# Kernel tuning notes

Hardware: AMD Instinct MI355X
Metric: run time of the kernel (lower is better)

Reference implementation:

```python
import jax, jax.numpy as jnp
import numpy as np

N_NODES = 50000
N_EDGES = 800000
IN_F, OUT_F = 128, 128
NUM_HEADS, QUERY_DIM = 3, 8


def setup_inputs() -> dict:
    key = jax.random.key(0)
    ks = jax.random.split(key, 8)
    scale = 1.0 / np.sqrt(IN_F)
    return {
        "x": jax.random.normal(ks[0], (N_NODES, IN_F), dtype=jnp.float32),
        "adj": jax.random.randint(ks[1], (2, N_EDGES), 0, N_NODES, dtype=jnp.int64),
        "Wq": jax.random.normal(ks[2], (QUERY_DIM * NUM_HEADS, IN_F), dtype=jnp.float32) * scale,
        "bq": jax.random.normal(ks[3], (QUERY_DIM * NUM_HEADS,), dtype=jnp.float32) * 0.01,
        "aw": jax.random.normal(ks[4], (NUM_HEADS, 2 * QUERY_DIM * NUM_HEADS), dtype=jnp.float32) * 0.1,
        "ab": jax.random.normal(ks[5], (NUM_HEADS,), dtype=jnp.float32) * 0.01,
        "lw": jax.random.normal(ks[6], (OUT_F, IN_F), dtype=jnp.float32) * scale,
        "lb": jax.random.normal(ks[7], (OUT_F,), dtype=jnp.float32) * 0.01,
    }


def reference(x, adj, Wq, bq, aw, ab, lw, lb):
    n = x.shape[0]
    s, r = adj[0], adj[1]
    # per-node query features: [N, H*Q]
    attr = x @ Wq.T + bq
    # per-edge attention logits from concat(sender, receiver): [E, H]
    e = jnp.concatenate((attr[s], attr[r]), axis=1) @ aw.T + ab
    # segment softmax over incoming edges of each receiver
    seg_max = jax.ops.segment_max(e, r, num_segments=n)  # [N, H]
    e = jnp.exp(e - jax.lax.stop_gradient(seg_max)[r])
    denom = jax.ops.segment_sum(e, r, num_segments=n)  # [N, H]
    alpha = e / jnp.maximum(denom[r], 1e-16)  # [E, H]
    # node value projection and attention-weighted aggregation
    h = x @ lw.T + lb  # [N, OUT_F]
    msg = h[s] * alpha.mean(axis=1, keepdims=True)  # [E, OUT_F]
    out = jax.ops.segment_sum(msg, r, num_segments=n)  # [N, OUT_F]
    return jax.nn.silu(out)
```

## Files before the change

kernel.cpp:

```cpp
#include <hip/hip_runtime.h>
#include <hip/hip_fp16.h>
#include <math.h>

#define N_NODES 50000
#define N_EDGES 800000
#define IN_F 128
#define OUT_F 128
#define NH 3
#define SCAN_NB ((N_NODES + 255) / 256)
#define NODE_NB ((N_NODES + 31) / 32)
#define NBH 32
#define EPB (N_EDGES / NBH)
#define QNODES (N_NODES / 4)
#define CQ_BLOCKS (NBH * 4)

typedef __attribute__((ext_vector_type(8))) _Float16 f16x8;
typedef __attribute__((ext_vector_type(4))) float f32x4;

__global__ __launch_bounds__(256) void weights_kernel(
    const float* __restrict__ Wq, const float* __restrict__ bq,
    const float* __restrict__ aw, const float* __restrict__ ab,
    const float* __restrict__ lw,
    _Float16* __restrict__ w2h, float* __restrict__ b2,
    _Float16* __restrict__ lwh, int* __restrict__ sync)
{
    int t = blockIdx.x * 256 + threadIdx.x;
    if (blockIdx.x == 0 && threadIdx.x < 8) sync[threadIdx.x] = 0;
    if (t < 16 * 128) {
        int prow = t >> 7;
        int i    = t & 127;
        int r = -1;
        if (prow < 3) r = prow;
        else if (prow >= 4 && prow < 7) r = prow - 1;
        if (r < 0) {
            w2h[prow * 128 + i] = (_Float16)0.0f;
        } else {
            int hh  = (r < 3) ? r : r - 3;
            int off = (r < 3) ? 0 : 24;
            const float* awr = aw + hh * 48 + off;
            float acc = 0.0f;
            #pragma unroll
            for (int q = 0; q < 24; q++) acc += awr[q] * Wq[q * 128 + i];
            w2h[prow * 128 + i] = (_Float16)acc;
            if (i == 0) {
                float b = 0.0f;
                #pragma unroll
                for (int q = 0; q < 24; q++) b += awr[q] * bq[q];
                if (r >= 3) b += ab[hh];
                b2[r] = b;
            }
        }
    }
    int u = t - 16 * 128;
    if (u >= 0 && u < 128 * 128) lwh[u] = (_Float16)lw[u];
}

__global__ __launch_bounds__(256) void node_count_kernel(
    const float* __restrict__ x, const _Float16* __restrict__ lwh,
    const float* __restrict__ lb, const _Float16* __restrict__ w2h,
    const float* __restrict__ b2, const int* __restrict__ adj,
    __half* __restrict__ h, float* __restrict__ as4, float* __restrict__ ar4,
    unsigned int* __restrict__ hist, unsigned short* __restrict__ rank)
{
    __shared__ __align__(16) unsigned int shmem[QNODES / 2];

    if (blockIdx.x < CQ_BLOCKS) {
        unsigned int* cnt = shmem;
        for (int i = threadIdx.x; i < QNODES / 2; i += 256) cnt[i] = 0;
        __syncthreads();
        const int c = blockIdx.x >> 2, q = blockIdx.x & 3;
        const int nlo = q * QNODES;
        const int e0 = c * EPB, e1 = e0 + EPB;
        for (int base = e0 + threadIdx.x; base < e1; base += 8 * 256) {
            int rs[8];
            #pragma unroll
            for (int u = 0; u < 8; u++) {
                int e = base + u * 256;
                rs[u] = (e < e1) ? adj[N_EDGES + e] : -1;
            }
            #pragma unroll
            for (int u = 0; u < 8; u++) {
                int e = base + u * 256;
                int lr = rs[u] - nlo;
                if ((unsigned)lr < (unsigned)QNODES) {
                    int sh = (lr & 1) * 16;
                    unsigned int old = atomicAdd(&cnt[lr >> 1], 1u << sh);
                    rank[e] = (unsigned short)(old >> sh);
                }
            }
        }
        __syncthreads();
        unsigned int* hb = hist + (size_t)c * (N_NODES / 2) + q * (QNODES / 2);
        for (int i = threadIdx.x; i < QNODES / 2; i += 256)
            hb[i] = cnt[i];
        return;
    }

    unsigned char* xs = (unsigned char*)shmem;
    const int tx = threadIdx.x;
    const int nb = (blockIdx.x - CQ_BLOCKS) * 32;

    #pragma unroll
    for (int it = 0; it < 2; it++) {
        int cc = it * 256 + tx;
        int node = cc >> 4, kc = cc & 15;
        int gn = nb + node;
        f16x8 v;
        if (gn < N_NODES) {
            const float4* xr = (const float4*)(x + (size_t)gn * 128 + kc * 8);
            float4 p = xr[0], qq = xr[1];
            v[0] = (_Float16)p.x;  v[1] = (_Float16)p.y;
            v[2] = (_Float16)p.z;  v[3] = (_Float16)p.w;
            v[4] = (_Float16)qq.x; v[5] = (_Float16)qq.y;
            v[6] = (_Float16)qq.z; v[7] = (_Float16)qq.w;
        } else {
            #pragma unroll
            for (int e = 0; e < 8; e++) v[e] = (_Float16)0.0f;
        }
        int byte = node * 256 + ((kc * 16) ^ ((node & 7) << 4));
        *(f16x8*)(xs + byte) = v;
    }
    __syncthreads();

    const int wave = tx >> 6, lane = tx & 63;
    const int l15 = lane & 15, lg = lane >> 4;

    f16x8 afr[2][4];
    #pragma unroll
    for (int m = 0; m < 2; m++) {
        int out = wave * 32 + m * 16 + l15;
        const f16x8* ar8 = (const f16x8*)(lwh + (size_t)out * 128);
        #pragma unroll
        for (int kk = 0; kk < 4; kk++)
            afr[m][kk] = ar8[kk * 4 + lg];
    }
    f16x8 a6[4];
    {
        const f16x8* w8 = (const f16x8*)(w2h + (size_t)l15 * 128);
        #pragma unroll
        for (int kk = 0; kk < 4; kk++) a6[kk] = w8[kk * 4 + lg];
    }

    f32x4 acc[2][2], acc6[2];
    #pragma unroll
    for (int m = 0; m < 2; m++)
        #pragma unroll
        for (int n = 0; n < 2; n++)
            acc[m][n] = (f32x4){0.f, 0.f, 0.f, 0.f};
    #pragma unroll
    for (int n = 0; n < 2; n++) acc6[n] = (f32x4){0.f, 0.f, 0.f, 0.f};

    #pragma unroll
    for (int kk = 0; kk < 4; kk++) {
        f16x8 bfr[2];
        #pragma unroll
        for (int n = 0; n < 2; n++) {
            int node = n * 16 + l15;
            int byte = node * 256 + ((kk * 64 + lg * 16) ^ ((node & 7) << 4));
            bfr[n] = *(const f16x8*)(xs + byte);
        }
        #pragma unroll
        for (int m = 0; m < 2; m++)
            #pragma unroll
            for (int n = 0; n < 2; n++)
                acc[m][n] = __builtin_amdgcn_mfma_f32_16x16x32_f16(
                    afr[m][kk], bfr[n], acc[m][n], 0, 0, 0);
        if (wave == 0) {
            #pragma unroll
            for (int n = 0; n < 2; n++)
                acc6[n] = __builtin_amdgcn_mfma_f32_16x16x32_f16(
                    a6[kk], bfr[n], acc6[n], 0, 0, 0);
        }
    }

    #pragma unroll
    for (int n = 0; n < 2; n++) {
        int gn = nb + n * 16 + l15;
        if (gn >= N_NODES) continue;
        #pragma unroll
        for (int m = 0; m < 2; m++) {
            int outb = wave * 32 + m * 16 + lg * 4;
            float4 lbv = *(const float4*)&lb[outb];
            __half2 p0 = __floats2half2_rn(acc[m][n].x + lbv.x, acc[m][n].y + lbv.y);
            __half2 p1 = __floats2half2_rn(acc[m][n].z + lbv.z, acc[m][n].w + lbv.w);
            int2 st;
            st.x = *(int*)&p0;
            st.y = *(int*)&p1;
            *(int2*)&h[(size_t)gn * 128 + outb] = st;
        }
    }

    if (wave == 0 && lg < 2) {
        float b0, bx, by;
        if (lg == 0) { b0 = b2[0]; bx = b2[1]; by = b2[2]; }
        else         { b0 = b2[3]; bx = b2[4]; by = b2[5]; }
        #pragma unroll
        for (int n = 0; n < 2; n++) {
            int gn = nb + n * 16 + l15;
            if (gn >= N_NODES) continue;
            float4 v = make_float4(acc6[n].x + b0, acc6[n].y + bx,
                                   acc6[n].z + by, 0.0f);
            if (lg == 0) *(float4*)&as4[(size_t)gn * 4] = v;
            else         *(float4*)&ar4[(size_t)gn * 4] = v;
        }
    }
}

__global__ __launch_bounds__(256) void scan_kernel(
    const unsigned int* __restrict__ hist, int* __restrict__ start,
    unsigned short* __restrict__ offs16,
    int* __restrict__ psum, int* __restrict__ poffs, int* __restrict__ sync)
{
    const int t = threadIdx.x, b = blockIdx.x;
    const int i = b * 256 + t;
    const int w = i >> 1, sh = (i & 1) * 16;
    int tot = 0;
    if (i < N_NODES) {
        for (int c = 0; c < NBH; c++)
            tot += (hist[(size_t)c * (N_NODES / 2) + w] >> sh) & 0xffff;
    }
    __shared__ int shm[256];
    shm[t] = tot;
    __syncthreads();
    #pragma unroll
    for (int off = 1; off < 256; off <<= 1) {
        int u = (t >= off) ? shm[t - off] : 0;
        __syncthreads();
        shm[t] += u;
        __syncthreads();
    }
    const int incl = shm[t];
    if (t == 255)
        __hip_atomic_store(&psum[b], incl, __ATOMIC_RELAXED,
                           __HIP_MEMORY_SCOPE_AGENT);
    __syncthreads();
    if (t == 0)
        __hip_atomic_fetch_add(&sync[0], 1, __ATOMIC_RELEASE,
                               __HIP_MEMORY_SCOPE_AGENT);

    if (b == 0) {
        if (t == 0)
            while (__hip_atomic_load(&sync[0], __ATOMIC_ACQUIRE,
                                     __HIP_MEMORY_SCOPE_AGENT) < SCAN_NB) {}
        __syncthreads();
        int pv = (t < SCAN_NB)
               ? __hip_atomic_load(&psum[t], __ATOMIC_RELAXED,
                                   __HIP_MEMORY_SCOPE_AGENT)
               : 0;
        shm[t] = pv;
        __syncthreads();
        #pragma unroll
        for (int off = 1; off < 256; off <<= 1) {
            int u = (t >= off) ? shm[t - off] : 0;
            __syncthreads();
            shm[t] += u;
            __syncthreads();
        }
        if (t < SCAN_NB)
            __hip_atomic_store(&poffs[t], shm[t] - pv, __ATOMIC_RELAXED,
                               __HIP_MEMORY_SCOPE_AGENT);
        __syncthreads();
        if (t == 0)
            __hip_atomic_store(&sync[1], 1, __ATOMIC_RELEASE,
                               __HIP_MEMORY_SCOPE_AGENT);
    }

    if (t == 0)
        while (__hip_atomic_load(&sync[1], __ATOMIC_ACQUIRE,
                                 __HIP_MEMORY_SCOPE_AGENT) == 0) {}
    __syncthreads();
    const int base = __hip_atomic_load(&poffs[b], __ATOMIC_RELAXED,
                                       __HIP_MEMORY_SCOPE_AGENT);
    if (i < N_NODES) {
        start[i] = base + incl - tot;
        int acc = 0;
        for (int c = 0; c < NBH; c++) {
            offs16[(size_t)c * N_NODES + i] = (unsigned short)acc;
            acc += (hist[(size_t)c * (N_NODES / 2) + w] >> sh) & 0xffff;
        }
    }
    if (i == N_NODES - 1) start[N_NODES] = base + incl;
}

__global__ __launch_bounds__(256) void fill_kernel(
    const int* __restrict__ adj, const int* __restrict__ start,
    const unsigned short* __restrict__ offs16,
    const unsigned short* __restrict__ rank,
    unsigned short* __restrict__ srcs)
{
    int e = blockIdx.x * 512 + threadIdx.x;
    #pragma unroll
    for (int u = 0; u < 2; u++, e += 256) {
        if (e < N_EDGES) {
            int r = adj[N_EDGES + e];
            int cb = e / EPB;
            int pos = start[r] + (int)offs16[(size_t)cb * N_NODES + r]
                    + (int)rank[e];
            srcs[pos] = (unsigned short)adj[e];
        }
    }
}

__global__ __launch_bounds__(256) void agg_kernel(
    const int* __restrict__ start, const unsigned short* __restrict__ srcs,
    const float4* __restrict__ as4, const float* __restrict__ ar4,
    const __half* __restrict__ h, float* __restrict__ out)
{
    const int wave = threadIdx.x >> 6;
    const int lane = threadIdx.x & 63;
    const int n = blockIdx.x * 4 + wave;
    if (n >= N_NODES) return;
    const int s0 = start[n], s1 = start[n + 1];
    const int deg = s1 - s0;

    __shared__ float sh_c[4][64];
    __shared__ int   sh_s[4][64];

    const float4 cr = *(const float4*)&ar4[(size_t)n * 4];
    const int quar = lane >> 4, l15 = lane & 15;
    const int4* hq = (const int4*)h;
    float a0 = 0.f, a1 = 0.f, a2 = 0.f, a3 = 0.f;
    float a4 = 0.f, a5 = 0.f, a6 = 0.f, a7 = 0.f;

    if (deg <= 64) {
        float e0 = 0.f, e1 = 0.f, e2 = 0.f;
        int s = 0;
        if (lane < deg) {
            s = srcs[s0 + lane];
            float4 a = as4[s];
            e0 = __expf(a.x + cr.x);
            e1 = __expf(a.y + cr.y);
            e2 = __expf(a.z + cr.z);
        }
        float p0 = e0, p1 = e1, p2 = e2;
        #pragma unroll
        for (int off = 32; off >= 1; off >>= 1) {
            p0 += __shfl_xor(p0, off);
            p1 += __shfl_xor(p1, off);
            p2 += __shfl_xor(p2, off);
        }
        const float i0 = (1.0f / 3.0f) / fmaxf(p0, 1e-30f);
        const float i1 = (1.0f / 3.0f) / fmaxf(p1, 1e-30f);
        const float i2 = (1.0f / 3.0f) / fmaxf(p2, 1e-30f);
        if (lane < deg) {
            sh_s[wave][lane] = s;
            sh_c[wave][lane] = e0 * i0 + e1 * i1 + e2 * i2;
        } else if (lane < deg + 3) {
            sh_s[wave][lane] = 0;
            sh_c[wave][lane] = 0.0f;
        }
        #pragma unroll 2
        for (int j = 0; j < deg; j += 4) {
            int jj = j + quar;
            float c = sh_c[wave][jj];
            int sj = sh_s[wave][jj];
            int4 hv = hq[(size_t)sj * 16 + l15];
            float2 f0 = __half22float2(*(const __half2*)&hv.x);
            float2 f1 = __half22float2(*(const __half2*)&hv.y);
            float2 f2 = __half22float2(*(const __half2*)&hv.z);
            float2 f3 = __half22float2(*(const __half2*)&hv.w);
            a0 = fmaf(f0.x, c, a0); a1 = fmaf(f0.y, c, a1);
            a2 = fmaf(f1.x, c, a2); a3 = fmaf(f1.y, c, a3);
            a4 = fmaf(f2.x, c, a4); a5 = fmaf(f2.y, c, a5);
            a6 = fmaf(f3.x, c, a6); a7 = fmaf(f3.y, c, a7);
        }
    } else {
        float p0 = 0.f, p1 = 0.f, p2 = 0.f;
        for (int k = s0 + lane; k < s1; k += 64) {
            float4 a = as4[srcs[k]];
            p0 += __expf(a.x + cr.x);
            p1 += __expf(a.y + cr.y);
            p2 += __expf(a.z + cr.z);
        }
        #pragma unroll
        for (int off = 32; off >= 1; off >>= 1) {
            p0 += __shfl_xor(p0, off);
            p1 += __shfl_xor(p1, off);
            p2 += __shfl_xor(p2, off);
        }
        const float i0 = (1.0f / 3.0f) / fmaxf(p0, 1e-30f);
        const float i1 = (1.0f / 3.0f) / fmaxf(p1, 1e-30f);
        const float i2 = (1.0f / 3.0f) / fmaxf(p2, 1e-30f);

        for (int cb = s0; cb < s1; cb += 64) {
            int cnt = min(64, s1 - cb);
            if (lane < cnt) {
                int s = srcs[cb + lane];
                float4 a = as4[s];
                sh_s[wave][lane] = s;
                sh_c[wave][lane] = __expf(a.x + cr.x) * i0
                                 + __expf(a.y + cr.y) * i1
                                 + __expf(a.z + cr.z) * i2;
            } else if (lane < cnt + 3) {
                sh_s[wave][lane] = 0;
                sh_c[wave][lane] = 0.0f;
            }
            #pragma unroll 2
            for (int j = 0; j < cnt; j += 4) {
                int jj = j + quar;
                float c = sh_c[wave][jj];
                int sj = sh_s[wave][jj];
                int4 hv = hq[(size_t)sj * 16 + l15];
                float2 f0 = __half22float2(*(const __half2*)&hv.x);
                float2 f1 = __half22float2(*(const __half2*)&hv.y);
                float2 f2 = __half22float2(*(const __half2*)&hv.z);
                float2 f3 = __half22float2(*(const __half2*)&hv.w);
                a0 = fmaf(f0.x, c, a0); a1 = fmaf(f0.y, c, a1);
                a2 = fmaf(f1.x, c, a2); a3 = fmaf(f1.y, c, a3);
                a4 = fmaf(f2.x, c, a4); a5 = fmaf(f2.y, c, a5);
                a6 = fmaf(f3.x, c, a6); a7 = fmaf(f3.y, c, a7);
            }
        }
    }

    a0 += __shfl_xor(a0, 16); a0 += __shfl_xor(a0, 32);
    a1 += __shfl_xor(a1, 16); a1 += __shfl_xor(a1, 32);
    a2 += __shfl_xor(a2, 16); a2 += __shfl_xor(a2, 32);
    a3 += __shfl_xor(a3, 16); a3 += __shfl_xor(a3, 32);
    a4 += __shfl_xor(a4, 16); a4 += __shfl_xor(a4, 32);
    a5 += __shfl_xor(a5, 16); a5 += __shfl_xor(a5, 32);
    a6 += __shfl_xor(a6, 16); a6 += __shfl_xor(a6, 32);
    a7 += __shfl_xor(a7, 16); a7 += __shfl_xor(a7, 32);

    if (quar == 0) {
        float4 o0, o1;
        o0.x = a0 / (1.0f + __expf(-a0));
        o0.y = a1 / (1.0f + __expf(-a1));
        o0.z = a2 / (1.0f + __expf(-a2));
        o0.w = a3 / (1.0f + __expf(-a3));
        o1.x = a4 / (1.0f + __expf(-a4));
        o1.y = a5 / (1.0f + __expf(-a5));
        o1.z = a6 / (1.0f + __expf(-a6));
        o1.w = a7 / (1.0f + __expf(-a7));
        *(float4*)&out[(size_t)n * 128 + l15 * 8] = o0;
        *(float4*)&out[(size_t)n * 128 + l15 * 8 + 4] = o1;
    }
}

extern "C" void kernel_launch(void* const* d_in, const int* in_sizes, int n_in,
                              void* d_out, int out_size, void* d_ws, size_t ws_size,
                              hipStream_t stream)
{
    const float* x  = (const float*)d_in[0];
    const int*   adj= (const int*)  d_in[1];
    const float* Wq = (const float*)d_in[2];
    const float* bq = (const float*)d_in[3];
    const float* aw = (const float*)d_in[4];
    const float* ab = (const float*)d_in[5];
    const float* lw = (const float*)d_in[6];
    const float* lb = (const float*)d_in[7];
    float* out = (float*)d_out;

    _Float16* w2h = (_Float16*)d_ws;
    float* b2     = (float*)(w2h + 2048);
    _Float16* lwh = (_Float16*)(b2 + 8);
    float* as4    = (float*)(lwh + 16384);
    float* ar4    = as4 + (size_t)N_NODES * 4;
    __half* h     = (__half*)(ar4 + (size_t)N_NODES * 4);
    int* start    = (int*)(h + (size_t)N_NODES * 128);
    int* sync     = start + (N_NODES + 1);
    unsigned int* hist = (unsigned int*)(sync + 8);
    unsigned short* offs16 = (unsigned short*)(hist + (size_t)NBH * (N_NODES / 2));
    unsigned short* rank   = offs16 + (size_t)NBH * N_NODES;
    unsigned short* srcs   = rank + N_EDGES;
    int* psum     = (int*)(srcs + N_EDGES);
    int* poffs    = psum + 256;

    weights_kernel<<<72, 256, 0, stream>>>(Wq, bq, aw, ab, lw, w2h, b2, lwh,
                                           sync);

    node_count_kernel<<<CQ_BLOCKS + NODE_NB, 256, 0, stream>>>(
        x, lwh, lb, w2h, b2, adj, h, as4, ar4, hist, rank);

    scan_kernel<<<SCAN_NB, 256, 0, stream>>>(hist, start, offs16,
                                             psum, poffs, sync);

    fill_kernel<<<(N_EDGES + 511) / 512, 256, 0, stream>>>(
        adj, start, offs16, rank, srcs);

    agg_kernel<<<(N_NODES + 3) / 4, 256, 0, stream>>>(
        start, srcs, (const float4*)as4, ar4, h, out);
}
```

Baseline: 114.1 us.

## Replace per-chunk shared-memory histograms with global atomic degree counts

Drops the 32-chunk by 4-quarter shared-memory histogram (packed 16-bit counters) and the per-chunk offset table. Receiver degrees are now counted with global atomicAdd on a deg array that the weights kernel zeroes, and the returned value serves as the edge's rank. This removes the 32-way histogram reduction in the scan, the offs16 writes, and the extra gather in the fill kernel. In exchange, 800K global atomics contend on a 50K-entry array, and the edge order inside each segment is no longer deterministic.

```diff
diff --git a/kernel.cpp b/kernel.cpp
--- a/kernel.cpp
+++ b/kernel.cpp
@@ -9,10 +9,8 @@
 #define NH 3
 #define SCAN_NB ((N_NODES + 255) / 256)
 #define NODE_NB ((N_NODES + 31) / 32)
-#define NBH 32
-#define EPB (N_EDGES / NBH)
-#define QNODES (N_NODES / 4)
-#define CQ_BLOCKS (NBH * 4)
+#define NCNT 128
+#define EPC (N_EDGES / NCNT)
 
 typedef __attribute__((ext_vector_type(8))) _Float16 f16x8;
 typedef __attribute__((ext_vector_type(4))) float f32x4;
@@ -22,10 +20,12 @@
     const float* __restrict__ aw, const float* __restrict__ ab,
     const float* __restrict__ lw,
     _Float16* __restrict__ w2h, float* __restrict__ b2,
-    _Float16* __restrict__ lwh, int* __restrict__ sync)
+    _Float16* __restrict__ lwh, int* __restrict__ sync,
+    int* __restrict__ deg)
 {
     int t = blockIdx.x * 256 + threadIdx.x;
     if (blockIdx.x == 0 && threadIdx.x < 8) sync[threadIdx.x] = 0;
+    for (int z = t; z < N_NODES; z += 72 * 256) deg[z] = 0;
     if (t < 16 * 128) {
         int prow = t >> 7;
         int i    = t & 127;
@@ -60,17 +60,12 @@
     const float* __restrict__ lb, const _Float16* __restrict__ w2h,
     const float* __restrict__ b2, const int* __restrict__ adj,
     __half* __restrict__ h, float* __restrict__ as4, float* __restrict__ ar4,
-    unsigned int* __restrict__ hist, unsigned short* __restrict__ rank)
-{
-    __shared__ __align__(16) unsigned int shmem[QNODES / 2];
-
-    if (blockIdx.x < CQ_BLOCKS) {
-        unsigned int* cnt = shmem;
-        for (int i = threadIdx.x; i < QNODES / 2; i += 256) cnt[i] = 0;
-        __syncthreads();
-        const int c = blockIdx.x >> 2, q = blockIdx.x & 3;
-        const int nlo = q * QNODES;
-        const int e0 = c * EPB, e1 = e0 + EPB;
+    int* __restrict__ deg, unsigned short* __restrict__ rank)
+{
+    __shared__ __align__(16) unsigned char xs[32 * 256];
+
+    if (blockIdx.x < NCNT) {
+        const int e0 = blockIdx.x * EPC, e1 = e0 + EPC;
         for (int base = e0 + threadIdx.x; base < e1; base += 8 * 256) {
             int rs[8];
             #pragma unroll
@@ -81,24 +76,17 @@
             #pragma unroll
             for (int u = 0; u < 8; u++) {
                 int e = base + u * 256;
-                int lr = rs[u] - nlo;
-                if ((unsigned)lr < (unsigned)QNODES) {
-                    int sh = (lr & 1) * 16;
-                    unsigned int old = atomicAdd(&cnt[lr >> 1], 1u << sh);
-                    rank[e] = (unsigned short)(old >> sh);
+                if (rs[u] >= 0) {
+                    int old = atomicAdd(&deg[rs[u]], 1);
+                    rank[e] = (unsigned short)old;
                 }
             }
         }
-        __syncthreads();
-        unsigned int* hb = hist + (size_t)c * (N_NODES / 2) + q * (QNODES / 2);
-        for (int i = threadIdx.x; i < QNODES / 2; i += 256)
-            hb[i] = cnt[i];
         return;
     }
 
-    unsigned char* xs = (unsigned char*)shmem;
     const int tx = threadIdx.x;
-    const int nb = (blockIdx.x - CQ_BLOCKS) * 32;
+    const int nb = (blockIdx.x - NCNT) * 32;
 
     #pragma unroll
     for (int it = 0; it < 2; it++) {
@@ -207,18 +195,12 @@
 }
 
 __global__ __launch_bounds__(256) void scan_kernel(
-    const unsigned int* __restrict__ hist, int* __restrict__ start,
-    unsigned short* __restrict__ offs16,
+    const int* __restrict__ deg, int* __restrict__ start,
     int* __restrict__ psum, int* __restrict__ poffs, int* __restrict__ sync)
 {
     const int t = threadIdx.x, b = blockIdx.x;
     const int i = b * 256 + t;
-    const int w = i >> 1, sh = (i & 1) * 16;
-    int tot = 0;
-    if (i < N_NODES) {
-        for (int c = 0; c < NBH; c++)
-            tot += (hist[(size_t)c * (N_NODES / 2) + w] >> sh) & 0xffff;
-    }
+    const int tot = (i < N_NODES) ? deg[i] : 0;
     __shared__ int shm[256];
     shm[t] = tot;
     __syncthreads();
@@ -271,20 +253,12 @@
     __syncthreads();
     const int base = __hip_atomic_load(&poffs[b], __ATOMIC_RELAXED,
                                        __HIP_MEMORY_SCOPE_AGENT);
-    if (i < N_NODES) {
-        start[i] = base + incl - tot;
-        int acc = 0;
-        for (int c = 0; c < NBH; c++) {
-            offs16[(size_t)c * N_NODES + i] = (unsigned short)acc;
-            acc += (hist[(size_t)c * (N_NODES / 2) + w] >> sh) & 0xffff;
-        }
-    }
+    if (i < N_NODES) start[i] = base + incl - tot;
     if (i == N_NODES - 1) start[N_NODES] = base + incl;
 }
 
 __global__ __launch_bounds__(256) void fill_kernel(
     const int* __restrict__ adj, const int* __restrict__ start,
-    const unsigned short* __restrict__ offs16,
     const unsigned short* __restrict__ rank,
     unsigned short* __restrict__ srcs)
 {
@@ -293,9 +267,7 @@
     for (int u = 0; u < 2; u++, e += 256) {
         if (e < N_EDGES) {
             int r = adj[N_EDGES + e];
-            int cb = e / EPB;
-            int pos = start[r] + (int)offs16[(size_t)cb * N_NODES + r]
-                    + (int)rank[e];
+            int pos = start[r] + (int)rank[e];
             srcs[pos] = (unsigned short)adj[e];
         }
     }
@@ -459,24 +431,22 @@
     __half* h     = (__half*)(ar4 + (size_t)N_NODES * 4);
     int* start    = (int*)(h + (size_t)N_NODES * 128);
     int* sync     = start + (N_NODES + 1);
-    unsigned int* hist = (unsigned int*)(sync + 8);
-    unsigned short* offs16 = (unsigned short*)(hist + (size_t)NBH * (N_NODES / 2));
-    unsigned short* rank   = offs16 + (size_t)NBH * N_NODES;
-    unsigned short* srcs   = rank + N_EDGES;
+    int* deg      = sync + 8;
+    unsigned short* rank = (unsigned short*)(deg + N_NODES);
+    unsigned short* srcs = rank + N_EDGES;
     int* psum     = (int*)(srcs + N_EDGES);
     int* poffs    = psum + 256;
 
     weights_kernel<<<72, 256, 0, stream>>>(Wq, bq, aw, ab, lw, w2h, b2, lwh,
-                                           sync);
-
-    node_count_kernel<<<CQ_BLOCKS + NODE_NB, 256, 0, stream>>>(
-        x, lwh, lb, w2h, b2, adj, h, as4, ar4, hist, rank);
-
-    scan_kernel<<<SCAN_NB, 256, 0, stream>>>(hist, start, offs16,
-                                             psum, poffs, sync);
+                                           sync, deg);
+
+    node_count_kernel<<<NCNT + NODE_NB, 256, 0, stream>>>(
+        x, lwh, lb, w2h, b2, adj, h, as4, ar4, deg, rank);
+
+    scan_kernel<<<SCAN_NB, 256, 0, stream>>>(deg, start, psum, poffs, sync);
 
     fill_kernel<<<(N_EDGES + 511) / 512, 256, 0, stream>>>(
-        adj, start, offs16, rank, srcs);
+        adj, start, rank, srcs);
 
     agg_kernel<<<(N_NODES + 3) / 4, 256, 0, stream>>>(
         start, srcs, (const float4*)as4, ar4, h, out);
```

Result: slower. 117.9 us (+3.4%).
